# Kernel tuning notes

Measured on AMD Instinct MI355X. Metric: run time of the kernel, lower is better.

Reference implementation:

```python
import jax, jax.numpy as jnp
import numpy as np

B, T = 64, 600
N_MEL = 80
ENC_POS = 512 + 32          # encoder_embedding_dim + positional_embedding_dim
PRENET = 256
RNN = 1024
RNN1_IN = PRENET + ENC_POS  # 800
PROJ_IN = RNN + ENC_POS     # 1568


def setup_inputs() -> dict:
    key = jax.random.key(0)
    ks = jax.random.split(key, 16)
    s = 0.02
    return {
        "duration_outputs": jax.random.normal(ks[0], (B, T, ENC_POS), jnp.float32),
        "decoder_inputs": jax.random.normal(ks[1], (B, N_MEL, T), jnp.float32),
        "memory_lengths": jax.random.randint(ks[2], (B,), 1, 200),
        # Prenet (bias=False)
        "Wp1": jax.random.normal(ks[3], (PRENET, N_MEL), jnp.float32) * s,
        "Wp2": jax.random.normal(ks[4], (PRENET, PRENET), jnp.float32) * s,
        # LSTMCell 1
        "W_ih1": jax.random.normal(ks[5], (4 * RNN, RNN1_IN), jnp.float32) * s,
        "W_hh1": jax.random.normal(ks[6], (4 * RNN, RNN), jnp.float32) * s,
        "b_ih1": jnp.zeros((4 * RNN,), jnp.float32),
        "b_hh1": jnp.zeros((4 * RNN,), jnp.float32),
        # LSTMCell 2
        "W_ih2": jax.random.normal(ks[7], (4 * RNN, RNN), jnp.float32) * s,
        "W_hh2": jax.random.normal(ks[8], (4 * RNN, RNN), jnp.float32) * s,
        "b_ih2": jnp.zeros((4 * RNN,), jnp.float32),
        "b_hh2": jnp.zeros((4 * RNN,), jnp.float32),
        # linear projection
        "Wproj": jax.random.normal(ks[9], (N_MEL, PROJ_IN), jnp.float32) * s,
        "bproj": jnp.zeros((N_MEL,), jnp.float32),
    }


def _lstm_cell(x, h, c, Wih, Whh, bih, bhh):
    gates = x @ Wih.T + bih + h @ Whh.T + bhh  # [B, 4*RNN]
    i, f, g, o = jnp.split(gates, 4, axis=-1)
    c_new = jax.nn.sigmoid(f) * c + jax.nn.sigmoid(i) * jnp.tanh(g)
    h_new = jax.nn.sigmoid(o) * jnp.tanh(c_new)
    return h_new, c_new


def _dropout(x, key, p=0.5):
    keep = jax.random.bernoulli(key, 1.0 - p, x.shape)
    return jnp.where(keep, x / (1.0 - p), 0.0)


def reference(duration_outputs, decoder_inputs, memory_lengths,
              Wp1, Wp2, W_ih1, W_hh1, b_ih1, b_hh1,
              W_ih2, W_hh2, b_ih2, b_hh2, Wproj, bproj):
    # parse_decoder_inputs: [B, n_mel, T] -> [T, B, n_mel] (n_frames_per_step=1)
    dec_in = jnp.transpose(decoder_inputs, (2, 0, 1))
    go = jnp.zeros((1, B, N_MEL), dec_in.dtype)
    dec_in = jnp.concatenate([go, dec_in], axis=0)  # [T+1, B, n_mel]

    # Prenet: F.dropout with training=True (always active); fixed keys for determinism
    dk1, dk2 = jax.random.split(jax.random.key(42))
    h = _dropout(jax.nn.relu(dec_in @ Wp1.T), dk1)
    h = _dropout(jax.nn.relu(h @ Wp2.T), dk2)  # [T+1, B, prenet]

    dur = jnp.transpose(duration_outputs, (1, 0, 2))  # [T, B, enc+pos]

    def step(carry, xs):
        h1, c1, h2, c2 = carry
        pn, du = xs
        x = jnp.concatenate([pn, du], axis=-1)
        h1, c1 = _lstm_cell(x, h1, c1, W_ih1, W_hh1, b_ih1, b_hh1)
        h2, c2 = _lstm_cell(h1, h2, c2, W_ih2, W_hh2, b_ih2, b_hh2)
        out = jnp.concatenate([h2, du], axis=-1) @ Wproj.T + bproj  # [B, n_mel]
        return (h1, c1, h2, c2), out

    z = jnp.zeros((B, RNN), jnp.float32)
    _, mel = jax.lax.scan(step, (z, z, z, z), (h[:T], dur))  # [T, B, n_mel]
    # stack -> transpose(0,1) -> view -> transpose(1,2): final [B, n_mel, T]
    return jnp.transpose(mel, (1, 2, 0))
```

## Files before the change

### kernel.cpp

```cpp
#include <hip/hip_runtime.h>
#include <hip/hip_bf16.h>
#include <stdint.h>


typedef short  bf16x8  __attribute__((ext_vector_type(8)));
typedef float  f32x16  __attribute__((ext_vector_type(16)));
typedef uint32_t u32x4 __attribute__((ext_vector_type(4)));

__device__ __forceinline__ uint32_t rotl32(uint32_t x, int r) {
  return (x << r) | (x >> (32 - r));
}

__device__ __forceinline__ void tf2x32(uint32_t k0, uint32_t k1,
                                       uint32_t x0, uint32_t x1,
                                       uint32_t& o0, uint32_t& o1) {
  uint32_t k2 = k0 ^ k1 ^ 0x1BD11BDAu;
  x0 += k0; x1 += k1;
#define TF_R(r) { x0 += x1; x1 = rotl32(x1, r); x1 ^= x0; }
  TF_R(13) TF_R(15) TF_R(26) TF_R(6)   x0 += k1; x1 += k2 + 1u;
  TF_R(17) TF_R(29) TF_R(16) TF_R(24)  x0 += k2; x1 += k0 + 2u;
  TF_R(13) TF_R(15) TF_R(26) TF_R(6)   x0 += k0; x1 += k1 + 3u;
  TF_R(17) TF_R(29) TF_R(16) TF_R(24)  x0 += k1; x1 += k2 + 4u;
  TF_R(13) TF_R(15) TF_R(26) TF_R(6)   x0 += k2; x1 += k0 + 5u;
#undef TF_R
  o0 = x0; o1 = x1;
}

__device__ __forceinline__ void dropout_keys(uint32_t& a1, uint32_t& b1,
                                             uint32_t& a2, uint32_t& b2) {
  uint32_t o0, o1, p0, p1;
  tf2x32(0u, 42u, 0u, 2u, o0, o1);
  tf2x32(0u, 42u, 1u, 3u, p0, p1);
  a1 = o0; b1 = p0;
  a2 = o1; b2 = p1;
}

__device__ __forceinline__ bool keep_mask(uint32_t ka, uint32_t kb, uint32_t e) {
  const uint32_t H = 4923392u;
  uint32_t o0, o1;
  if (e < H) { tf2x32(ka, kb, e, e + H, o0, o1); return o0 < 0x80000000u; }
  else       { tf2x32(ka, kb, e - H, e, o0, o1); return o1 < 0x80000000u; }
}

__device__ __forceinline__ float sigf(float x)  { return 1.f / (1.f + __expf(-x)); }
__device__ __forceinline__ float tanhf2(float x){ return 2.f / (1.f + __expf(-2.f * x)) - 1.f; }

__device__ __forceinline__ short bf16bits(float f) {
  __hip_bfloat16 h = __float2bfloat16(f);
  short s; __builtin_memcpy(&s, &h, 2);
  return s;
}
__device__ __forceinline__ float bflo(uint32_t u) {
  uint32_t x = u << 16; float f; __builtin_memcpy(&f, &x, 4); return f;
}
__device__ __forceinline__ float bfhi(uint32_t u) {
  uint32_t x = u & 0xffff0000u; float f; __builtin_memcpy(&f, &x, 4); return f;
}

__device__ __forceinline__ void st_u32_a(void* p, uint32_t v) {
  __hip_atomic_store((uint32_t*)p, v, __ATOMIC_RELAXED, __HIP_MEMORY_SCOPE_AGENT);
}

__device__ __forceinline__ void ld8_mall(const __hip_bfloat16* p, bf16x8 (&d)[8]) {
  asm volatile(
      "global_load_dwordx4 %0, %8, off sc0 sc1\n\t"
      "global_load_dwordx4 %1, %8, off offset:32 sc0 sc1\n\t"
      "global_load_dwordx4 %2, %8, off offset:64 sc0 sc1\n\t"
      "global_load_dwordx4 %3, %8, off offset:96 sc0 sc1\n\t"
      "global_load_dwordx4 %4, %8, off offset:128 sc0 sc1\n\t"
      "global_load_dwordx4 %5, %8, off offset:160 sc0 sc1\n\t"
      "global_load_dwordx4 %6, %8, off offset:192 sc0 sc1\n\t"
      "global_load_dwordx4 %7, %8, off offset:224 sc0 sc1\n\t"
      "s_waitcnt vmcnt(0)"
      : "=&v"(d[0]), "=&v"(d[1]), "=&v"(d[2]), "=&v"(d[3]),
        "=&v"(d[4]), "=&v"(d[5]), "=&v"(d[6]), "=&v"(d[7])
      : "v"(p) : "memory");
}
__device__ __forceinline__ void ld4_mall4_issue(const uint32_t* p0, const uint32_t* p1,
                                                const uint32_t* p2, const uint32_t* p3,
                                                uint32_t (&d)[4]) {
  asm volatile(
      "global_load_dword %0, %4, off sc0 sc1\n\t"
      "global_load_dword %1, %5, off sc0 sc1\n\t"
      "global_load_dword %2, %6, off sc0 sc1\n\t"
      "global_load_dword %3, %7, off sc0 sc1"
      : "=&v"(d[0]), "=&v"(d[1]), "=&v"(d[2]), "=&v"(d[3])
      : "v"(p0), "v"(p1), "v"(p2), "v"(p3) : "memory");
}
__device__ __forceinline__ void ld4_s512_issue(const __hip_bfloat16* p,
                                               uint32_t (&d)[4]) {
  asm volatile(
      "global_load_dword %0, %4, off sc0 sc1\n\t"
      "global_load_dword %1, %4, off offset:512 sc0 sc1\n\t"
      "global_load_dword %2, %4, off offset:1024 sc0 sc1\n\t"
      "global_load_dword %3, %4, off offset:1536 sc0 sc1"
      : "=&v"(d[0]), "=&v"(d[1]), "=&v"(d[2]), "=&v"(d[3])
      : "v"(p) : "memory");
}
__device__ __forceinline__ void ld4_pin(uint32_t (&d)[4]) {
  asm volatile("s_waitcnt vmcnt(0)"
               : "+v"(d[0]), "+v"(d[1]), "+v"(d[2]), "+v"(d[3])
               :: "memory");
  __builtin_amdgcn_sched_barrier(0);
}
__device__ __forceinline__ u32x4 ld_flags16(const uint32_t* p) {
  u32x4 d;
  asm volatile(
      "global_load_dwordx4 %0, %1, off sc0 sc1\n\t"
      "s_waitcnt vmcnt(0)"
      : "=&v"(d) : "v"(p) : "memory");
  return d;
}

__global__ void prenet1_kernel(const float* __restrict__ dec,
                               const float* __restrict__ Wp1,
                               float* __restrict__ pn1) {
  const int t = blockIdx.x;
  const int tid = threadIdx.x;
  __shared__ float          sdec[64][81];
  __shared__ __hip_bfloat16 sw1[256][80];
  for (int idx = tid; idx < 64 * 80; idx += 256) {
    int b = idx / 80, m = idx - b * 80;
    sdec[b][m] = (t == 0) ? 0.f : dec[b * 48000 + m * 600 + (t - 1)];
  }
  for (int idx = tid; idx < 256 * 80; idx += 256) {
    int j = idx / 80, k = idx - j * 80;
    sw1[j][k] = __float2bfloat16(Wp1[idx]);
  }
  __syncthreads();
  uint32_t ka, kb, ka2, kb2;
  dropout_keys(ka, kb, ka2, kb2);
  const int b  = tid & 63;
  const int jg = tid >> 6;
  for (int jj = 0; jj < 64; ++jj) {
    const int j = jg * 64 + jj;
    float acc = 0.f;
    #pragma unroll
    for (int k = 0; k < 80; ++k)
      acc += sdec[b][k] * __bfloat162float(sw1[j][k]);
    const uint32_t e = (uint32_t)((t * 64 + b) * 256 + j);
    pn1[(t * 64 + b) * 256 + j] =
        keep_mask(ka, kb, e) ? 2.f * fmaxf(acc, 0.f) : 0.f;
  }
}

__global__ void prenet2_kernel(const float* __restrict__ pn1,
                               const float* __restrict__ Wp2,
                               __hip_bfloat16* __restrict__ X) {
  const int t  = blockIdx.x;
  const int j0 = blockIdx.y * 32;
  const int tid = threadIdx.x;
  __shared__ __hip_bfloat16 sact[64][258];
  __shared__ __hip_bfloat16 sw[32][256];
  for (int idx = tid; idx < 64 * 256; idx += 256) {
    int b = idx >> 8, k = idx & 255;
    sact[b][k] = __float2bfloat16(pn1[(t * 64 + b) * 256 + k]);
  }
  for (int idx = tid; idx < 32 * 256; idx += 256) {
    int r = idx >> 8, k = idx & 255;
    sw[r][k] = __float2bfloat16(Wp2[(j0 + r) * 256 + k]);
  }
  __syncthreads();
  uint32_t ka, kb, ka2, kb2;
  dropout_keys(ka, kb, ka2, kb2);
  const int b  = tid & 63;
  const int jg = tid >> 6;
  float acc[8];
  #pragma unroll
  for (int c = 0; c < 8; ++c) acc[c] = 0.f;
  for (int k = 0; k < 256; ++k) {
    const float a = __bfloat162float(sact[b][k]);
    #pragma unroll
    for (int c = 0; c < 8; ++c)
      acc[c] += a * __bfloat162float(sw[jg * 8 + c][k]);
  }
  #pragma unroll
  for (int c = 0; c < 8; ++c) {
    const int j = j0 + jg * 8 + c;
    const uint32_t e = (uint32_t)((t * 64 + b) * 256 + j);
    const float v = keep_mask(ka2, kb2, e) ? 2.f * fmaxf(acc[c], 0.f) : 0.f;
    X[(t * 64 + b) * 1024 + j] = __float2bfloat16(v);
  }
}

__global__ void xfill_kernel(const float* __restrict__ dur,
                             __hip_bfloat16* __restrict__ X) {
  const int idx = blockIdx.x * 256 + threadIdx.x;
  const int t  = idx / 49152;
  const int r  = idx - t * 49152;
  const int b  = r / 768;
  const int kk = r - b * 768;
  const float v = (kk < 544) ? dur[(b * 600 + t) * 544 + kk] : 0.f;
  X[(t * 64 + b) * 1024 + 256 + kk] = __float2bfloat16(v);
}

__global__ void wprojcvt_kernel(const float* __restrict__ W,
                                __hip_bfloat16* __restrict__ Wb) {
  const int idx = blockIdx.x * 256 + threadIdx.x;
  Wb[idx] = __float2bfloat16(W[idx]);
}

__launch_bounds__(512, 2)
__global__ void persist_kernel(
    const float* __restrict__ Wih1, const float* __restrict__ Whh1,
    const float* __restrict__ bih1, const float* __restrict__ bhh1,
    const float* __restrict__ Wih2, const float* __restrict__ Whh2,
    const float* __restrict__ bih2, const float* __restrict__ bhh2,
    const __hip_bfloat16* __restrict__ WprojB, const float* __restrict__ bproj,
    const __hip_bfloat16* __restrict__ Xbuf,
    uint32_t* __restrict__ P0, uint32_t* __restrict__ P1,
    __hip_bfloat16* __restrict__ h1buf, __hip_bfloat16* __restrict__ h2buf,
    uint32_t* __restrict__ flags,
    float* __restrict__ out) {
  const int bid  = blockIdx.x;
  const int role = bid >> 6;
  const int sub  = bid & 63;
  const int tid  = threadIdx.x;
  const int wave = tid >> 6;
  const int lane = tid & 63;
  const int mh   = wave & 1;
  const int kseg = wave >> 1;

  __shared__ float pbuf4[4][2][32][65];
  __shared__ float sbuf[8][8];

  const float* Wsrc = (role == 0) ? Wih1 : (role == 1) ? Whh1
                    : (role == 2) ? Wih2 : Whh2;
  const int Ksrc  = (role == 0) ? 800 : 1024;
  const int nrow  = lane & 31;
  const int khalf = (lane >> 5) * 8;
  bf16x8 bfr[16][2];
  #pragma unroll
  for (int ks = 0; ks < 16; ++ks) {
    #pragma unroll
    for (int nt = 0; nt < 2; ++nt) {
      const int nloc = nt * 32 + nrow;
      const int g = (role == 1 || role == 3)
                  ? ((nloc >> 4) * 1024 + sub * 16 + (nloc & 15))
                  : (sub * 64 + nloc);
      const int k0 = kseg * 256 + ks * 16 + khalf;
      bf16x8 v;
      if (k0 + 8 <= Ksrc) {
        const float* wp = Wsrc + (size_t)g * (size_t)Ksrc + k0;
        #pragma unroll
        for (int j = 0; j < 8; ++j) v[j] = bf16bits(wp[j]);
      } else {
        #pragma unroll
        for (int j = 0; j < 8; ++j) v[j] = (short)0;
      }
      bfr[ks][nt] = v;
    }
  }

  float breg[8];
  if (role == 0 || role == 2) {
    const float* bi = (role == 0) ? bih1 : bih2;
    const float* bh = (role == 0) ? bhh1 : bhh2;
    const int c0 = (tid * 8) & 63;
    #pragma unroll
    for (int j = 0; j < 8; ++j) {
      const int g = sub * 64 + c0 + j;
      breg[j] = bi[g] + bh[g];
    }
  }

  float cst[2] = {0.f, 0.f};
  const int brow = mh * 32 + (lane & 31);
  const int c0p = (bid & 15) * 5;
  const int bp  = (bid >> 4) * 4 + (tid >> 7);
  const int kl  = tid & 127;

  for (int tau = 0; tau < 604; ++tau) {
    const int sl = tau & 1;
    const bool active =
        (role == 0) ? (tau <= 599) :
        (role == 1) ? (tau >= 1 && tau <= 600) :
        (role == 2) ? (tau >= 2 && tau <= 601) :
                      (tau >= 3 && tau <= 602);
    const bool pact = (tau >= 4);

    uint32_t hreg[4];
    if (pact) {
      ld4_s512_issue(h2buf + sl * 65536 + bp * 1024 + kl * 2, hreg);
    }

    f32x16 acc0, acc1;
    #pragma unroll
    for (int i = 0; i < 16; ++i) { acc0[i] = 0.f; acc1[i] = 0.f; }

    uint32_t pg4[4] = {0u, 0u, 0u, 0u};

    if (active) {
      if (role == 0) {
        const bf16x8* ap = reinterpret_cast<const bf16x8*>(
            Xbuf + (size_t)tau * 65536 + brow * 1024 + kseg * 256 + khalf);
        #pragma unroll
        for (int ks = 0; ks < 16; ++ks) {
          const bf16x8 a = ap[ks * 2];
          acc0 = __builtin_amdgcn_mfma_f32_32x32x16_bf16(a, bfr[ks][0], acc0, 0, 0, 0);
          acc1 = __builtin_amdgcn_mfma_f32_32x32x16_bf16(a, bfr[ks][1], acc1, 0, 0, 0);
        }
      } else {
        if (role & 1) {
          const uint32_t* Psrc = ((role == 1) ? P0 : P1) + ((tau + 1) & 1) * 131072;
          const int hcp = (tid & 7) * 2;
          const int pb  = tid >> 3;
          const uint32_t* q = Psrc + ((pb * 4096 + sub * 16 + hcp) >> 1);
          ld4_mall4_issue(q, q + 512, q + 1024, q + 1536, pg4);
        }
        const __hip_bfloat16* Asrc =
            ((role == 3) ? h2buf : h1buf) + sl * 65536;
        const __hip_bfloat16* abase = Asrc + brow * 1024 + kseg * 256 + khalf;
        bf16x8 A[8];
        ld8_mall(abase, A);
        #pragma unroll
        for (int ks = 0; ks < 8; ++ks) {
          acc0 = __builtin_amdgcn_mfma_f32_32x32x16_bf16(A[ks], bfr[ks][0], acc0, 0, 0, 0);
          acc1 = __builtin_amdgcn_mfma_f32_32x32x16_bf16(A[ks], bfr[ks][1], acc1, 0, 0, 0);
        }
        ld8_mall(abase + 128, A);
        #pragma unroll
        for (int ks = 0; ks < 8; ++ks) {
          acc0 = __builtin_amdgcn_mfma_f32_32x32x16_bf16(A[ks], bfr[ks + 8][0], acc0, 0, 0, 0);
          acc1 = __builtin_amdgcn_mfma_f32_32x32x16_bf16(A[ks], bfr[ks + 8][1], acc1, 0, 0, 0);
        }
      }
    }
    if (active) {
      #pragma unroll
      for (int reg = 0; reg < 16; ++reg) {
        const int mrow = (reg & 3) + 8 * (reg >> 2) + 4 * (lane >> 5);
        const int col  = lane & 31;
        pbuf4[kseg][mh][mrow][col]      = acc0[reg];
        pbuf4[kseg][mh][mrow][col + 32] = acc1[reg];
      }
    }
    __syncthreads();
    if (active) {
      if (role == 0 || role == 2) {
        uint32_t* Pd = ((role == 0) ? P0 : P1) + sl * 131072;
        const int i0 = tid * 8;
        const int b  = i0 >> 6;
        const int c0 = i0 & 63;
        uint32_t* dst = Pd + ((b * 4096 + sub * 64 + c0) >> 1);
        const int m = b & 31, mb = b >> 5;
        const float* q0 = &pbuf4[0][mb][m][0];
        const float* q1 = &pbuf4[1][mb][m][0];
        const float* q2 = &pbuf4[2][mb][m][0];
        const float* q3 = &pbuf4[3][mb][m][0];
        #pragma unroll
        for (int j = 0; j < 4; ++j) {
          const int ca = c0 + 2 * j, cb = c0 + 2 * j + 1;
          const float va = ((q0[ca] + q1[ca]) + q2[ca]) + q3[ca] + breg[2 * j];
          const float vb = ((q0[cb] + q1[cb]) + q2[cb]) + q3[cb] + breg[2 * j + 1];
          const uint32_t lo = (uint32_t)(uint16_t)bf16bits(va);
          const uint32_t hi = (uint32_t)(uint16_t)bf16bits(vb);
          st_u32_a(dst + j, lo | (hi << 16));
        }
      } else {
        ld4_pin(pg4);
        __hip_bfloat16* hdst =
            ((role == 1) ? h1buf : h2buf) + ((tau + 1) & 1) * 65536;
        const int hcp = (tid & 7) * 2;
        const int b   = tid >> 3;
        const int m = b & 31, mb = b >> 5;
        const float* q0 = &pbuf4[0][mb][m][0];
        const float* q1 = &pbuf4[1][mb][m][0];
        const float* q2 = &pbuf4[2][mb][m][0];
        const float* q3 = &pbuf4[3][mb][m][0];
#define SUM4(idx) ((((q0[idx] + q1[idx]) + q2[idx]) + q3[idx]))
        const float gi0 = SUM4(hcp)      + bflo(pg4[0]), gi1 = SUM4(hcp + 1)      + bfhi(pg4[0]);
        const float gf0 = SUM4(16 + hcp) + bflo(pg4[1]), gf1 = SUM4(16 + hcp + 1) + bfhi(pg4[1]);
        const float gg0 = SUM4(32 + hcp) + bflo(pg4[2]), gg1 = SUM4(32 + hcp + 1) + bfhi(pg4[2]);
        const float go0 = SUM4(48 + hcp) + bflo(pg4[3]), go1 = SUM4(48 + hcp + 1) + bfhi(pg4[3]);
#undef SUM4
        const float c0n = sigf(gf0) * cst[0] + sigf(gi0) * tanhf2(gg0);
        const float c1n = sigf(gf1) * cst[1] + sigf(gi1) * tanhf2(gg1);
        cst[0] = c0n; cst[1] = c1n;
        const uint32_t h0 = (uint32_t)(uint16_t)bf16bits(sigf(go0) * tanhf2(c0n));
        const uint32_t h1v = (uint32_t)(uint16_t)bf16bits(sigf(go1) * tanhf2(c1n));
        st_u32_a(hdst + b * 1024 + sub * 16 + hcp, h0 | (h1v << 16));
      }
    }
    __syncthreads();
    if (tid == 0) st_u32_a(flags + (size_t)tau * 256 + bid, 1u);

    if (pact) {
      ld4_pin(hreg);
      const __hip_bfloat16* xs = Xbuf + (size_t)(tau - 4) * 65536;
      float pj[5];
      #pragma unroll
      for (int c = 0; c < 5; ++c) pj[c] = 0.f;
      #pragma unroll
      for (int i = 0; i < 4; ++i) {
        const int k2 = kl * 2 + i * 256;
        const float a0 = bflo(hreg[i]), a1 = bfhi(hreg[i]);
        #pragma unroll
        for (int c = 0; c < 5; ++c) {
          const uint32_t w = *(const uint32_t*)(WprojB + (c0p + c) * 1568 + k2);
          pj[c] += a0 * bflo(w) + a1 * bfhi(w);
        }
      }
      for (int k2 = kl * 2 + 1024; k2 < 1568; k2 += 256) {
        const uint32_t u = *(const uint32_t*)(xs + bp * 1024 + (k2 - 768));
        const float a0 = bflo(u), a1 = bfhi(u);
        #pragma unroll
        for (int c = 0; c < 5; ++c) {
          const uint32_t w = *(const uint32_t*)(WprojB + (c0p + c) * 1568 + k2);
          pj[c] += a0 * bflo(w) + a1 * bfhi(w);
        }
      }
      #pragma unroll
      for (int c = 0; c < 5; ++c) {
        #pragma unroll
        for (int off = 32; off > 0; off >>= 1)
          pj[c] += __shfl_xor(pj[c], off, 64);
      }
      if (lane == 0) {
        #pragma unroll
        for (int c = 0; c < 5; ++c) sbuf[wave][c] = pj[c];
      }
    }
    __syncthreads();
    if (pact && ((wave & 1) == 0) && lane == 0) {
      const int b = (bid >> 4) * 4 + (wave >> 1);
      #pragma unroll
      for (int c = 0; c < 5; ++c)
        out[b * 48000 + (c0p + c) * 600 + (tau - 4)] =
            sbuf[wave][c] + sbuf[wave + 1][c] + bproj[c0p + c];
    }
    if (wave == 0) {
      const uint32_t* f = flags + (size_t)tau * 256 + lane * 4;
      for (;;) {
        u32x4 a = ld_flags16(f);
        if (__all((int)(a[0] & a[1] & a[2] & a[3]))) break;
        __builtin_amdgcn_s_sleep(2);
      }
    }
    __syncthreads();
  }
}

extern "C" void kernel_launch(void* const* d_in, const int* in_sizes, int n_in,
                              void* d_out, int out_size, void* d_ws, size_t ws_size,
                              hipStream_t stream) {
  (void)in_sizes; (void)n_in; (void)out_size; (void)ws_size;
  const float* dur   = (const float*)d_in[0];
  const float* dec   = (const float*)d_in[1];
  const float* Wp1   = (const float*)d_in[3];
  const float* Wp2   = (const float*)d_in[4];
  const float* Wih1  = (const float*)d_in[5];
  const float* Whh1  = (const float*)d_in[6];
  const float* bih1  = (const float*)d_in[7];
  const float* bhh1  = (const float*)d_in[8];
  const float* Wih2  = (const float*)d_in[9];
  const float* Whh2  = (const float*)d_in[10];
  const float* bih2  = (const float*)d_in[11];
  const float* bhh2  = (const float*)d_in[12];
  const float* Wproj = (const float*)d_in[13];
  const float* bproj = (const float*)d_in[14];

  char* ws = (char*)d_ws;
  __hip_bfloat16* X    = (__hip_bfloat16*)(ws + 0);
  __hip_bfloat16* WpjB = (__hip_bfloat16*)(ws + 78643200);
  char*           comm = ws + 78894080;
  uint32_t*       flags= (uint32_t*)(comm + 0);
  __hip_bfloat16* h1   = (__hip_bfloat16*)(comm + 618496);
  __hip_bfloat16* h2   = (__hip_bfloat16*)(comm + 880640);
  uint32_t*       P0   = (uint32_t*)(comm + 1142784);
  uint32_t*       P1   = (uint32_t*)(comm + 2191360);
  float*          pn1  = (float*)(ws + 78894080);

  prenet1_kernel<<<600, 256, 0, stream>>>(dec, Wp1, pn1);
  prenet2_kernel<<<dim3(600, 8), 256, 0, stream>>>(pn1, Wp2, X);
  hipMemsetAsync(comm, 0, 3239936, stream);
  xfill_kernel<<<115200, 256, 0, stream>>>(dur, X);
  wprojcvt_kernel<<<490, 256, 0, stream>>>(Wproj, WpjB);
  persist_kernel<<<256, 512, 0, stream>>>(Wih1, Whh1, bih1, bhh1,
                                          Wih2, Whh2, bih2, bhh2,
                                          WpjB, bproj, X, P0, P1, h1, h2,
                                          flags, (float*)d_out);
}
```

Measured before the change: 6.140 ms.

## Replace global all-block barrier with role-specific dependency waits

Drops the per-step wait that made every block poll all 256 flags after each step. Each role now waits only on the flag subsets from the previous step that it actually depends on, and a new projread flag array lets role 3 confirm that h2 readers have finished before it overwrites data. The aim is to cut global barrier latency on the sequential recurrent critical path. The cost is more complex cross-block synchronisation, a larger zeroed comm region, and a risk of races if a dependency was missed.

```diff
diff --git a/kernel.cpp b/kernel.cpp
--- a/kernel.cpp
+++ b/kernel.cpp
@@ -111,6 +111,24 @@
       : "=&v"(d) : "v"(p) : "memory");
   return d;
 }
+__device__ __forceinline__ void ld_flags2(const uint32_t* p0, const uint32_t* p1,
+                                          u32x4& a, u32x4& b) {
+  asm volatile(
+      "global_load_dwordx4 %0, %2, off sc0 sc1\n\t"
+      "global_load_dwordx4 %1, %3, off sc0 sc1\n\t"
+      "s_waitcnt vmcnt(0)"
+      : "=&v"(a), "=&v"(b) : "v"(p0), "v"(p1) : "memory");
+}
+__device__ __forceinline__ void ld_flags3(const uint32_t* p0, const uint32_t* p1,
+                                          const uint32_t* p2,
+                                          u32x4& a, u32x4& b, u32x4& c) {
+  asm volatile(
+      "global_load_dwordx4 %0, %3, off sc0 sc1\n\t"
+      "global_load_dwordx4 %1, %4, off sc0 sc1\n\t"
+      "global_load_dwordx4 %2, %5, off sc0 sc1\n\t"
+      "s_waitcnt vmcnt(0)"
+      : "=&v"(a), "=&v"(b), "=&v"(c) : "v"(p0), "v"(p1), "v"(p2) : "memory");
+}
 
 __global__ void prenet1_kernel(const float* __restrict__ dec,
                                const float* __restrict__ Wp1,
@@ -211,6 +229,7 @@
     uint32_t* __restrict__ P0, uint32_t* __restrict__ P1,
     __hip_bfloat16* __restrict__ h1buf, __hip_bfloat16* __restrict__ h2buf,
     uint32_t* __restrict__ flags,
+    uint32_t* __restrict__ projread,
     float* __restrict__ out) {
   const int bid  = blockIdx.x;
   const int role = bid >> 6;
@@ -279,6 +298,45 @@
                       (tau >= 3 && tau <= 602);
     const bool pact = (tau >= 4);
 
+    if (tau > 0) {
+      if (wave == 0) {
+        const uint32_t* prow = flags + (size_t)(tau - 1) * 256;
+        if (role == 1) {
+          const uint32_t* f = prow + lane * 4;
+          for (;;) {
+            u32x4 a = ld_flags16(f);
+            if (__all((int)(a[0] & a[1] & a[2] & a[3]))) break;
+            __builtin_amdgcn_s_sleep(2);
+          }
+        } else if (role == 3) {
+          const uint32_t* f0 = prow + 128 + (lane & 15) * 4;
+          const uint32_t* f1 = prow + 192 + (lane & 15) * 4;
+          const uint32_t* f2 = projread + (size_t)(tau - 1) * 256 + lane * 4;
+          for (;;) {
+            u32x4 a, b, c;
+            ld_flags3(f0, f1, f2, a, b, c);
+            const int ok = (int)((a[0] & a[1] & a[2] & a[3]) &
+                                 (b[0] & b[1] & b[2] & b[3]) &
+                                 (c[0] & c[1] & c[2] & c[3]));
+            if (__all(ok)) break;
+            __builtin_amdgcn_s_sleep(2);
+          }
+        } else {
+          const uint32_t* f0 = prow + 64 + (lane & 15) * 4;
+          const uint32_t* f1 = prow + 192 + (lane & 15) * 4;
+          for (;;) {
+            u32x4 a, b;
+            ld_flags2(f0, f1, a, b);
+            const int ok = (int)((a[0] & a[1] & a[2] & a[3]) &
+                                 (b[0] & b[1] & b[2] & b[3]));
+            if (__all(ok)) break;
+            __builtin_amdgcn_s_sleep(2);
+          }
+        }
+      }
+      __syncthreads();
+    }
+
     uint32_t hreg[4];
     if (pact) {
       ld4_s512_issue(h2buf + sl * 65536 + bp * 1024 + kl * 2, hreg);
@@ -336,6 +394,7 @@
       }
     }
     __syncthreads();
+    if (tid == 0) st_u32_a(projread + (size_t)tau * 256 + bid, 1u);
     if (active) {
       if (role == 0 || role == 2) {
         uint32_t* Pd = ((role == 0) ? P0 : P1) + sl * 131072;
@@ -429,15 +488,6 @@
         out[b * 48000 + (c0p + c) * 600 + (tau - 4)] =
             sbuf[wave][c] + sbuf[wave + 1][c] + bproj[c0p + c];
     }
-    if (wave == 0) {
-      const uint32_t* f = flags + (size_t)tau * 256 + lane * 4;
-      for (;;) {
-        u32x4 a = ld_flags16(f);
-        if (__all((int)(a[0] & a[1] & a[2] & a[3]))) break;
-        __builtin_amdgcn_s_sleep(2);
-      }
-    }
-    __syncthreads();
   }
 }
 
@@ -469,15 +519,16 @@
   __hip_bfloat16* h2   = (__hip_bfloat16*)(comm + 880640);
   uint32_t*       P0   = (uint32_t*)(comm + 1142784);
   uint32_t*       P1   = (uint32_t*)(comm + 2191360);
+  uint32_t*       prj  = (uint32_t*)(comm + 3239936);
   float*          pn1  = (float*)(ws + 78894080);
 
   prenet1_kernel<<<600, 256, 0, stream>>>(dec, Wp1, pn1);
   prenet2_kernel<<<dim3(600, 8), 256, 0, stream>>>(pn1, Wp2, X);
-  hipMemsetAsync(comm, 0, 3239936, stream);
+  hipMemsetAsync(comm, 0, 3858432, stream);
   xfill_kernel<<<115200, 256, 0, stream>>>(dur, X);
   wprojcvt_kernel<<<490, 256, 0, stream>>>(Wproj, WpjB);
   persist_kernel<<<256, 512, 0, stream>>>(Wih1, Whh1, bih1, bhh1,
                                           Wih2, Whh2, bih2, bhh2,
                                           WpjB, bproj, X, P0, P1, h1, h2,
-                                          flags, (float*)d_out);
-}
+                                          flags, prj, (float*)d_out);
+}
```

Result: no change. 6.188 ms (+0.8%).
